# Performance work log

Hardware: AMD Instinct MI355X
Metric: run time of the kernel (lower is better)

The kernel has to match this reference:

```python
import jax, jax.numpy as jnp
import numpy as np

EMB = 300      # LEN_EMB_VECTOR
FH, FO = 200, 200
GH, GO = 200, 200
HH, HO = 200, 3

def _mlp2(x, w1, b1, w2, b2):
    # relu(Linear) -> relu(Linear), torch Linear: y = x @ W.T + b
    h = jax.nn.relu(x @ w1.T + b1)
    return jax.nn.relu(h @ w2.T + b2)

def setup_inputs() -> dict:
    key = jax.random.key(0)
    ks = jax.random.split(key, 16)
    L1, L2 = 8192, 8192
    def lin(k, out_d, in_d):
        kw, kb = jax.random.split(k)
        s = 1.0 / np.sqrt(in_d)
        w = jax.random.uniform(kw, (out_d, in_d), jnp.float32, -s, s)
        b = jax.random.uniform(kb, (out_d,), jnp.float32, -s, s)
        return w, b
    F_w1, F_b1 = lin(ks[0], FH, EMB)
    F_w2, F_b2 = lin(ks[1], FO, FH)
    G_w1, G_b1 = lin(ks[2], GH, 2 * EMB)
    G_w2, G_b2 = lin(ks[3], GO, GH)
    H_w1, H_b1 = lin(ks[4], HH, 2 * GO)
    H_w2, H_b2 = lin(ks[5], HO, HH)
    sen1 = jax.random.normal(ks[6], (L1, EMB), jnp.float32)
    sen2 = jax.random.normal(ks[7], (L2, EMB), jnp.float32)
    return {"sen1": sen1, "sen2": sen2,
            "F_w1": F_w1, "F_b1": F_b1, "F_w2": F_w2, "F_b2": F_b2,
            "G_w1": G_w1, "G_b1": G_b1, "G_w2": G_w2, "G_b2": G_b2,
            "H_w1": H_w1, "H_b1": H_b1, "H_w2": H_w2, "H_b2": H_b2}

def reference(sen1, sen2, F_w1, F_b1, F_w2, F_b2,
              G_w1, G_b1, G_w2, G_b2, H_w1, H_b1, H_w2, H_b2):
    # F projection of every token in both sentences
    Fa = _mlp2(sen1, F_w1, F_b1, F_w2, F_b2)   # [L1, 200]
    Fb = _mlp2(sen2, F_w1, F_b1, F_w2, F_b2)   # [L2, 200]
    # E matrix of dot products: e_ij = Fa_i . Fb_j
    E = jnp.einsum('id,jd->ij', Fa, Fb)        # [L1, L2]
    # beta_i = softmax over j of E[i, :] applied to sen2
    beta = jax.nn.softmax(E, axis=1) @ sen2    # [L1, EMB]
    # alpha_j = softmax over i of E[:, j] applied to sen1
    alpha = jax.nn.softmax(E, axis=0).T @ sen1 # [L2, EMB]
    # G comparison
    v1 = _mlp2(jnp.concatenate([sen1, beta], axis=-1), G_w1, G_b1, G_w2, G_b2)   # [L1, 200]
    v2 = _mlp2(jnp.concatenate([sen2, alpha], axis=-1), G_w1, G_b1, G_w2, G_b2)  # [L2, 200]
    # aggregate: elementwise sums over tokens, then H classifier with softmax
    hx = jnp.concatenate([v1.sum(axis=0), v2.sum(axis=0)])  # [400]
    logits = jax.nn.relu(hx @ H_w1.T + H_b1) @ H_w2.T + H_b2  # [3]
    return jax.nn.softmax(logits)
```

## Files before the change

kernel.cpp:

```cpp
#include <hip/hip_runtime.h>

typedef __attribute__((ext_vector_type(8))) short short8;
typedef __attribute__((ext_vector_type(4))) float f32x4;

__device__ inline ushort f2bf(float f) {
    union { float f; unsigned u; } v{f};
    unsigned r = v.u + 0x7FFF + ((v.u >> 16) & 1);
    return (ushort)(r >> 16);
}
__device__ inline float bf2f(ushort u) {
    union { unsigned u; float f; } v;
    v.u = ((unsigned)u) << 16;
    return v.f;
}

__device__ inline void gload_lds16(const void* g, void* l) {
    __builtin_amdgcn_global_load_lds(
        (const __attribute__((address_space(1))) unsigned int*)(uintptr_t)g,
        (__attribute__((address_space(3))) unsigned int*)(uintptr_t)l,
        16, 0, 0);
}

__global__ __launch_bounds__(256) void convert_sen_kernel(
    const float* __restrict__ s1, const float* __restrict__ s2,
    ushort* __restrict__ Senb, ushort* __restrict__ St1, ushort* __restrict__ St2)
{
    const float* X = blockIdx.z ? s2 : s1;
    ushort* Xt = blockIdx.z ? St2 : St1;
    ushort* Sb = Senb + (size_t)blockIdx.z * 8192 * 320;
    __shared__ float t[64][65];
    const int r0 = blockIdx.x * 64, c0 = blockIdx.y * 64;
    const int tc = threadIdx.x & 63, tr = threadIdx.x >> 6;
    for (int rr = tr; rr < 64; rr += 4) {
        int c = c0 + tc;
        float v = (c < 300) ? X[(size_t)(r0 + rr) * 300 + c] : 0.f;
        t[rr][tc] = v;
        if (c < 320) Sb[(size_t)(r0 + rr) * 320 + c] = f2bf(v);
    }
    __syncthreads();
    for (int rr = tr; rr < 64; rr += 4) {
        int oc = c0 + rr;
        if (oc < 320)
            Xt[(size_t)oc * 8192 + r0 + tc] = f2bf(t[tc][rr]);
    }
}

__global__ __launch_bounds__(256) void convert_weights_kernel(
    const float* __restrict__ W0, const float* __restrict__ b0,
    const float* __restrict__ W1, const float* __restrict__ b1,
    const float* __restrict__ W2, const float* __restrict__ b2,
    const float* __restrict__ W3, const float* __restrict__ b3,
    ushort* __restrict__ Wb0, float* __restrict__ bp0,
    ushort* __restrict__ Wb1, float* __restrict__ bp1,
    ushort* __restrict__ Wb2, float* __restrict__ bp2,
    ushort* __restrict__ Wb3, float* __restrict__ bp3)
{
    const int id = blockIdx.x;
    const int mat = id / 224, n = id % 224;
    if (mat == 2) {
        for (int k = threadIdx.x; k < 640; k += 256) {
            float v = 0.f;
            if (n < 200) {
                if (k < 320) { if (k < 300) v = W2[(size_t)n * 600 + k]; }
                else { int cc = k - 320; if (cc < 300) v = W2[(size_t)n * 600 + 300 + cc]; }
            }
            Wb2[(size_t)n * 640 + k] = f2bf(v);
        }
        if (threadIdx.x == 0) bp2[n] = (n < 200) ? b2[n] : 0.f;
        return;
    }
    const float* W; const float* b; ushort* Wb; float* bp; int N, K, KP;
    if (mat == 0)      { W = W0; b = b0; Wb = Wb0; bp = bp0; N = 200; K = 300; KP = 320; }
    else if (mat == 1) { W = W1; b = b1; Wb = Wb1; bp = bp1; N = 200; K = 200; KP = 224; }
    else               { W = W3; b = b3; Wb = Wb3; bp = bp3; N = 200; K = 200; KP = 224; }
    for (int k = threadIdx.x; k < KP; k += 256)
        Wb[(size_t)n * KP + k] = (n < N && k < K) ? f2bf(W[(size_t)n * K + k]) : (ushort)0;
    if (threadIdx.x == 0) bp[n] = (n < N) ? b[n] : 0.f;
}

__global__ __launch_bounds__(64) void mlp2_kernel(
    const ushort* __restrict__ X, int KP1,
    const ushort* __restrict__ W1, const float* __restrict__ b1,
    const ushort* __restrict__ W2, const float* __restrict__ b2,
    ushort* __restrict__ Ybf)
{
    const int r0 = blockIdx.x * 16;
    const int lane = threadIdx.x;
    const int lr = lane & 15, lg = lane >> 4;

    __shared__ __align__(16) ushort Y1[16][232];

    f32x4 a1[14];
#pragma unroll
    for (int t = 0; t < 14; ++t) a1[t] = f32x4{0.f, 0.f, 0.f, 0.f};

    const ushort* Xrow = X + (size_t)(r0 + lr) * KP1 + lg * 8;
    const ushort* W1r  = W1 + (size_t)lr * KP1 + lg * 8;
    for (int k0 = 0; k0 < KP1; k0 += 32) {
        short8 a = *(const short8*)(Xrow + k0);
#pragma unroll
        for (int t = 0; t < 14; ++t) {
            short8 bfr = *(const short8*)(W1r + (size_t)t * 16 * KP1 + k0);
            a1[t] = __builtin_amdgcn_mfma_f32_16x16x32_bf16(a, bfr, a1[t], 0, 0, 0);
        }
    }
#pragma unroll
    for (int t = 0; t < 14; ++t) {
        int col = t * 16 + lr;
        float bv = b1[col];
#pragma unroll
        for (int rr = 0; rr < 4; ++rr)
            Y1[lg * 4 + rr][col] = f2bf(fmaxf(a1[t][rr] + bv, 0.f));
    }
    __syncthreads();

    f32x4 a2[14];
#pragma unroll
    for (int t = 0; t < 14; ++t) a2[t] = f32x4{0.f, 0.f, 0.f, 0.f};
    const ushort* W2r = W2 + (size_t)lr * 224 + lg * 8;
    for (int k0 = 0; k0 < 224; k0 += 32) {
        short8 a = *(const short8*)&Y1[lr][lg * 8 + k0];
#pragma unroll
        for (int t = 0; t < 14; ++t) {
            short8 bfr = *(const short8*)(W2r + (size_t)t * 16 * 224 + k0);
            a2[t] = __builtin_amdgcn_mfma_f32_16x16x32_bf16(a, bfr, a2[t], 0, 0, 0);
        }
    }
#pragma unroll
    for (int t = 0; t < 14; ++t) {
        int col = t * 16 + lr;
        float bv = b2[col];
#pragma unroll
        for (int rr = 0; rr < 4; ++rr) {
            int row = r0 + lg * 4 + rr;
            Ybf[(size_t)row * 224 + col] = f2bf(fmaxf(a2[t][rr] + bv, 0.f));
        }
    }
}

__global__ __launch_bounds__(64) void gmlp2_kernel(
    const ushort* __restrict__ Senb,
    const ushort* __restrict__ Pacc, const float* __restrict__ Dpart,
    const ushort* __restrict__ W1, const float* __restrict__ b1,
    const ushort* __restrict__ W2, const float* __restrict__ b2,
    float* __restrict__ Part)
{
    const int r0 = blockIdx.x * 16;
    const int lane = threadIdx.x;
    const int lr = lane & 15, lg = lane >> 4;
    const int row = r0 + lr;

    __shared__ __align__(16) ushort Y1[16][232];

    const float inv = 1.f / (Dpart[row] + Dpart[16384 + row]);
    const ushort* pa = Pacc + (size_t)row * 320;
    const ushort* pb = pa + (size_t)16384 * 320;

    f32x4 a1[14];
#pragma unroll
    for (int t = 0; t < 14; ++t) a1[t] = f32x4{0.f, 0.f, 0.f, 0.f};

    const ushort* Xrow = Senb + (size_t)row * 320 + lg * 8;
    const ushort* W1r  = W1 + (size_t)lr * 640 + lg * 8;
    for (int k0 = 0; k0 < 640; k0 += 32) {
        short8 a;
        if (k0 < 320) {
            a = *(const short8*)(Xrow + k0);
        } else {
            int kk = k0 - 320 + lg * 8;
            short8 x = *(const short8*)(pa + kk);
            short8 y = *(const short8*)(pb + kk);
#pragma unroll
            for (int m = 0; m < 8; ++m)
                a[m] = (short)f2bf((bf2f((ushort)x[m]) + bf2f((ushort)y[m])) * inv);
        }
#pragma unroll
        for (int t = 0; t < 14; ++t) {
            short8 bfr = *(const short8*)(W1r + (size_t)t * 16 * 640 + k0);
            a1[t] = __builtin_amdgcn_mfma_f32_16x16x32_bf16(a, bfr, a1[t], 0, 0, 0);
        }
    }
#pragma unroll
    for (int t = 0; t < 14; ++t) {
        int col = t * 16 + lr;
        float bv = b1[col];
#pragma unroll
        for (int rr = 0; rr < 4; ++rr)
            Y1[lg * 4 + rr][col] = f2bf(fmaxf(a1[t][rr] + bv, 0.f));
    }
    __syncthreads();

    f32x4 a2[14];
#pragma unroll
    for (int t = 0; t < 14; ++t) a2[t] = f32x4{0.f, 0.f, 0.f, 0.f};
    const ushort* W2r = W2 + (size_t)lr * 224 + lg * 8;
    for (int k0 = 0; k0 < 224; k0 += 32) {
        short8 a = *(const short8*)&Y1[lr][lg * 8 + k0];
#pragma unroll
        for (int t = 0; t < 14; ++t) {
            short8 bfr = *(const short8*)(W2r + (size_t)t * 16 * 224 + k0);
            a2[t] = __builtin_amdgcn_mfma_f32_16x16x32_bf16(a, bfr, a2[t], 0, 0, 0);
        }
    }
#pragma unroll
    for (int t = 0; t < 14; ++t) {
        int col = t * 16 + lr;
        if (col < 200) {
            float bv = b2[col];
            float s = 0.f;
#pragma unroll
            for (int rr = 0; rr < 4; ++rr)
                s += fmaxf(a2[t][rr] + bv, 0.f);
            s += __shfl_xor(s, 16);
            s += __shfl_xor(s, 32);
            if (lg == 0)
                Part[(size_t)blockIdx.x * 200 + col] = s;
        }
    }
}

__global__ __launch_bounds__(512, 2) void attend_mfma_kernel(
    const ushort* __restrict__ FaFb, const ushort* __restrict__ St1,
    const ushort* __restrict__ St2, ushort* __restrict__ Pacc,
    float* __restrict__ Dpart)
{
    const int b = blockIdx.x;
    const int it  = b & 63;
    const int jh  = (b >> 6) & 1;
    const int dir = b >> 7;
    const ushort* A  = FaFb + (dir ? (size_t)8192 * 224 : 0);
    const ushort* B  = FaFb + (dir ? 0 : (size_t)8192 * 224);
    const ushort* St = dir ? St1 : St2;
    const int ib = it * 128;
    const int jo = jh * 4096;

    const int tid = threadIdx.x;
    const int w = tid >> 6;
    const int wi = w >> 1, wj = w & 1;
    const int dq = w & 3,  ih = w >> 2;
    const int lane = tid & 63;
    const int lr = lane & 15, lg = lane >> 4;

    __shared__ __align__(16) ushort Bl[2][28 * 512];
    __shared__ __align__(16) ushort Sl[2][40 * 512];
    __shared__ __align__(16) ushort Pl[128][76];
    __shared__ float dled[8][32];

    f32x4 acc[4][5];
#pragma unroll
    for (int s = 0; s < 4; ++s)
#pragma unroll
        for (int t = 0; t < 5; ++t) acc[s][t] = f32x4{0.f, 0.f, 0.f, 0.f};
    float dsum[2] = {0.f, 0.f};

    short8 afr[2][7];
#pragma unroll
    for (int si = 0; si < 2; ++si) {
        const ushort* Ar = A + (size_t)(ib + wi * 32 + si * 16 + lr) * 224 + lg * 8;
#pragma unroll
        for (int k = 0; k < 7; ++k) afr[si][k] = *(const short8*)(Ar + k * 32);
    }

    const int nB = (w < 4) ? 4 : 3;
    const int pB = (w < 4) ? (w * 4) : (16 + (w - 4) * 3);
    int boff[4];
#pragma unroll
    for (int q = 0; q < 4; ++q) {
        int p = pB + q;
        boff[q] = ((p / 7) * 16 + lr) * 448 + ((p % 7) * 32 + lg * 8) * 2;
    }
    const char* Bb = (const char*)B + (size_t)jo * 448;

    int soff[5];
#pragma unroll
    for (int q = 0; q < 5; ++q) {
        int p = w * 5 + q;
        int srow = p * 8 + (lane >> 3);
        int sl = (lane & 7) ^ (srow & 7);
        soff[q] = srow * 16384 + sl * 16;
    }
    const char* Sb = (const char*)St + (size_t)jo * 2;

    int prow[5], prow7[5];
#pragma unroll
    for (int t = 0; t < 5; ++t) {
        prow[t] = (dq * 80 + t * 16 + lr) * 128;
        prow7[t] = (dq * 80 + t * 16 + lr) & 7;
    }

#pragma unroll
    for (int q = 0; q < 4; ++q)
        if (q < nB) gload_lds16(Bb + boff[q], &Bl[0][(pB + q) * 512]);
#pragma unroll
    for (int q = 0; q < 5; ++q)
        gload_lds16(Sb + soff[q], &Sl[0][(w * 5 + q) * 512]);
    __syncthreads();

    int buf = 0;
    for (int jb = 0; jb < 4096; jb += 64, buf ^= 1) {
        f32x4 e[2][2];
#pragma unroll
        for (int si = 0; si < 2; ++si)
#pragma unroll
            for (int jt = 0; jt < 2; ++jt) e[si][jt] = f32x4{0.f, 0.f, 0.f, 0.f};
        __builtin_amdgcn_s_setprio(1);
#pragma unroll
        for (int kk = 0; kk < 7; ++kk) {
            short8 b0 = *(const short8*)&Bl[buf][((2 * wj + 0) * 7 + kk) * 512 + lane * 8];
            short8 b1 = *(const short8*)&Bl[buf][((2 * wj + 1) * 7 + kk) * 512 + lane * 8];
            e[0][0] = __builtin_amdgcn_mfma_f32_16x16x32_bf16(b0, afr[0][kk], e[0][0], 0, 0, 0);
            e[1][0] = __builtin_amdgcn_mfma_f32_16x16x32_bf16(b0, afr[1][kk], e[1][0], 0, 0, 0);
            e[0][1] = __builtin_amdgcn_mfma_f32_16x16x32_bf16(b1, afr[0][kk], e[0][1], 0, 0, 0);
            e[1][1] = __builtin_amdgcn_mfma_f32_16x16x32_bf16(b1, afr[1][kk], e[1][1], 0, 0, 0);
        }
        __builtin_amdgcn_s_setprio(0);

#pragma unroll
        for (int si = 0; si < 2; ++si) {
#pragma unroll
            for (int jt = 0; jt < 2; ++jt) {
                float x0 = __expf(e[si][jt][0]);
                float x1 = __expf(e[si][jt][1]);
                float x2 = __expf(e[si][jt][2]);
                float x3 = __expf(e[si][jt][3]);
                dsum[si] += (x0 + x1) + (x2 + x3);
                uint2 pk;
                pk.x = (unsigned)f2bf(x0) | ((unsigned)f2bf(x1) << 16);
                pk.y = (unsigned)f2bf(x2) | ((unsigned)f2bf(x3) << 16);
                *(uint2*)&Pl[wi * 32 + si * 16 + lr][wj * 32 + jt * 16 + lg * 4] = pk;
            }
        }
        __syncthreads();

        if (jb + 64 < 4096) {
            const char* Bn = Bb + (size_t)(jb + 64) * 448;
            const char* Sn = Sb + (size_t)(jb + 64) * 2;
#pragma unroll
            for (int q = 0; q < 4; ++q)
                if (q < nB) gload_lds16(Bn + boff[q], &Bl[buf ^ 1][(pB + q) * 512]);
#pragma unroll
            for (int q = 0; q < 5; ++q)
                gload_lds16(Sn + soff[q], &Sl[buf ^ 1][(w * 5 + q) * 512]);
        }

#pragma unroll
        for (int h = 0; h < 2; ++h) {
            short8 pf[4];
#pragma unroll
            for (int s = 0; s < 4; ++s)
                pf[s] = *(const short8*)&Pl[ih * 64 + s * 16 + lr][h * 32 + lg * 8];
            short8 st[5];
#pragma unroll
            for (int t = 0; t < 5; ++t) {
                int sl = ((h << 2) | lg) ^ prow7[t];
                st[t] = *(const short8*)((const char*)Sl[buf] + prow[t] + (sl << 4));
            }
            __builtin_amdgcn_s_setprio(1);
#pragma unroll
            for (int s = 0; s < 4; ++s)
#pragma unroll
                for (int t = 0; t < 5; ++t)
                    acc[s][t] = __builtin_amdgcn_mfma_f32_16x16x32_bf16(pf[s], st[t], acc[s][t], 0, 0, 0);
            __builtin_amdgcn_s_setprio(0);
        }
        __syncthreads();
    }

#pragma unroll
    for (int si = 0; si < 2; ++si) {
        dsum[si] += __shfl_xor(dsum[si], 16);
        dsum[si] += __shfl_xor(dsum[si], 32);
    }
    if (lg == 0) {
#pragma unroll
        for (int si = 0; si < 2; ++si)
            dled[w][si * 16 + lr] = dsum[si];
    }
    __syncthreads();

    if (tid < 128) {
        int wi2 = tid >> 5, idx = tid & 31;
        Dpart[(size_t)jh * 16384 + dir * 8192 + ib + tid] =
            dled[wi2 * 2][idx] + dled[wi2 * 2 + 1][idx];
    }

    ushort* Pb = Pacc + ((size_t)jh * 16384 + dir * 8192 + ib + ih * 64) * 320;
#pragma unroll
    for (int t = 0; t < 5; ++t) {
        int d = dq * 80 + t * 16 + lr;
#pragma unroll
        for (int s = 0; s < 4; ++s)
#pragma unroll
            for (int r = 0; r < 4; ++r)
                Pb[(size_t)(s * 16 + lg * 4 + r) * 320 + d] = f2bf(acc[s][t][r]);
    }
}

__global__ __launch_bounds__(256) void colsum_part_kernel(
    const float* __restrict__ Part, float* __restrict__ hsum)
{
    const int c = blockIdx.x;
    const int base = (c < 200) ? 0 : 512;
    const int col = c % 200;
    float s = 0.f;
    for (int p = threadIdx.x; p < 512; p += 256)
        s += Part[(size_t)(base + p) * 200 + col];
    __shared__ float red[256];
    red[threadIdx.x] = s;
    __syncthreads();
    for (int off = 128; off > 0; off >>= 1) {
        if (threadIdx.x < off) red[threadIdx.x] += red[threadIdx.x + off];
        __syncthreads();
    }
    if (threadIdx.x == 0) hsum[c] = red[0];
}

__global__ __launch_bounds__(256) void head_kernel(
    const float* __restrict__ hsum,
    const float* __restrict__ Hw1, const float* __restrict__ Hb1,
    const float* __restrict__ Hw2, const float* __restrict__ Hb2,
    float* __restrict__ out)
{
    __shared__ float hx[400];
    __shared__ float hr[200];
    __shared__ float lg[3];
    const int t = threadIdx.x;
    for (int i = t; i < 400; i += 256) hx[i] = hsum[i];
    __syncthreads();
    if (t < 200) {
        float a = Hb1[t];
        for (int k = 0; k < 400; ++k) a = fmaf(hx[k], Hw1[t * 400 + k], a);
        hr[t] = fmaxf(a, 0.f);
    }
    __syncthreads();
    if (t < 3) {
        float a = Hb2[t];
        for (int k = 0; k < 200; ++k) a = fmaf(hr[k], Hw2[t * 200 + k], a);
        lg[t] = a;
    }
    __syncthreads();
    if (t == 0) {
        float m = fmaxf(lg[0], fmaxf(lg[1], lg[2]));
        float e0 = __expf(lg[0] - m);
        float e1 = __expf(lg[1] - m);
        float e2 = __expf(lg[2] - m);
        float s = e0 + e1 + e2;
        out[0] = e0 / s;
        out[1] = e1 / s;
        out[2] = e2 / s;
    }
}

extern "C" void kernel_launch(void* const* d_in, const int* in_sizes, int n_in,
                              void* d_out, int out_size, void* d_ws, size_t ws_size,
                              hipStream_t stream)
{
    const float* sen1 = (const float*)d_in[0];
    const float* sen2 = (const float*)d_in[1];
    const float* F_w1 = (const float*)d_in[2];
    const float* F_b1 = (const float*)d_in[3];
    const float* F_w2 = (const float*)d_in[4];
    const float* F_b2 = (const float*)d_in[5];
    const float* G_w1 = (const float*)d_in[6];
    const float* G_b1 = (const float*)d_in[7];
    const float* G_w2 = (const float*)d_in[8];
    const float* G_b2 = (const float*)d_in[9];
    const float* H_w1 = (const float*)d_in[10];
    const float* H_b1 = (const float*)d_in[11];
    const float* H_w2 = (const float*)d_in[12];
    const float* H_b2 = (const float*)d_in[13];
    float* out = (float*)d_out;

    const int L = 8192;
    char* p = (char*)d_ws;
    ushort* St1  = (ushort*)p; p += (size_t)320 * L * 2;
    ushort* St2  = (ushort*)p; p += (size_t)320 * L * 2;
    ushort* Senb = (ushort*)p; p += (size_t)2 * L * 320 * 2;
    ushort* FaFb = (ushort*)p; p += (size_t)2 * L * 224 * 2;
    ushort* WbF1 = (ushort*)p; p += (size_t)224 * 320 * 2;
    ushort* WbF2 = (ushort*)p; p += (size_t)224 * 224 * 2;
    ushort* WbG1 = (ushort*)p; p += (size_t)224 * 640 * 2;
    ushort* WbG2 = (ushort*)p; p += (size_t)224 * 224 * 2;
    float*  bpF1 = (float*)p;  p += 224 * 4;
    float*  bpF2 = (float*)p;  p += 224 * 4;
    float*  bpG1 = (float*)p;  p += 224 * 4;
    float*  bpG2 = (float*)p;  p += 224 * 4;
    float*  hsum = (float*)p;  p += 400 * 4;
    ushort* Pacc = (ushort*)p; p += (size_t)2 * 16384 * 320 * 2;
    float*  Dpart= (float*)p;  p += (size_t)2 * 16384 * 4;
    float*  Part = (float*)p;  p += (size_t)1024 * 200 * 4;

    dim3 blk256(256);

    hipLaunchKernelGGL(convert_sen_kernel, dim3(L / 64, 5, 2), blk256, 0, stream,
                       sen1, sen2, Senb, St1, St2);
    hipLaunchKernelGGL(convert_weights_kernel, dim3(4 * 224), blk256, 0, stream,
                       F_w1, F_b1, F_w2, F_b2, G_w1, G_b1, G_w2, G_b2,
                       WbF1, bpF1, WbF2, bpF2, WbG1, bpG1, WbG2, bpG2);

    hipLaunchKernelGGL(mlp2_kernel, dim3(2 * L / 16), dim3(64), 0, stream,
                       Senb, 320, WbF1, bpF1, WbF2, bpF2, FaFb);

    hipLaunchKernelGGL(attend_mfma_kernel, dim3(256), dim3(512), 0, stream,
                       FaFb, St1, St2, Pacc, Dpart);

    hipLaunchKernelGGL(gmlp2_kernel, dim3(2 * L / 16), dim3(64), 0, stream,
                       Senb, Pacc, Dpart, WbG1, bpG1, WbG2, bpG2, Part);

    hipLaunchKernelGGL(colsum_part_kernel, dim3(400), blk256, 0, stream, Part, hsum);
    hipLaunchKernelGGL(head_kernel, dim3(1), blk256, 0, stream,
                       hsum, H_w1, H_b1, H_w2, H_b2, out);
}
```

Before: 275.9 us.

## Split MLP K-dimension across two waves and merge prep/tail kernels

The F and G two-layer MLP kernels now run two wavefronts per block, each covering half of the K dimension. Partial sums are exchanged through shared memory, rounded to bf16, before bias and ReLU. The two conversion kernels are merged into one launch, and the column-sum and head kernels are merged into a single 1024-thread tail kernel. The aim is more parallelism in the latency-bound MLPs and fewer launches, at the cost of extra syncs and bf16 rounding of the partial sums.

```diff
diff --git a/kernel.cpp b/kernel.cpp
--- a/kernel.cpp
+++ b/kernel.cpp
@@ -21,15 +21,51 @@
         16, 0, 0);
 }
 
-__global__ __launch_bounds__(256) void convert_sen_kernel(
+__global__ __launch_bounds__(256) void prep_kernel(
     const float* __restrict__ s1, const float* __restrict__ s2,
-    ushort* __restrict__ Senb, ushort* __restrict__ St1, ushort* __restrict__ St2)
+    const float* __restrict__ W0, const float* __restrict__ b0,
+    const float* __restrict__ W1, const float* __restrict__ b1,
+    const float* __restrict__ W2, const float* __restrict__ b2,
+    const float* __restrict__ W3, const float* __restrict__ b3,
+    ushort* __restrict__ Senb, ushort* __restrict__ St1, ushort* __restrict__ St2,
+    ushort* __restrict__ Wb0, float* __restrict__ bp0,
+    ushort* __restrict__ Wb1, float* __restrict__ bp1,
+    ushort* __restrict__ Wb2, float* __restrict__ bp2,
+    ushort* __restrict__ Wb3, float* __restrict__ bp3)
 {
-    const float* X = blockIdx.z ? s2 : s1;
-    ushort* Xt = blockIdx.z ? St2 : St1;
-    ushort* Sb = Senb + (size_t)blockIdx.z * 8192 * 320;
+    const int bid = blockIdx.x;
+    if (bid < 896) {
+        const int mat = bid / 224, n = bid % 224;
+        if (mat == 2) {
+            for (int k = threadIdx.x; k < 640; k += 256) {
+                float v = 0.f;
+                if (n < 200) {
+                    if (k < 320) { if (k < 300) v = W2[(size_t)n * 600 + k]; }
+                    else { int cc = k - 320; if (cc < 300) v = W2[(size_t)n * 600 + 300 + cc]; }
+                }
+                Wb2[(size_t)n * 640 + k] = f2bf(v);
+            }
+            if (threadIdx.x == 0) bp2[n] = (n < 200) ? b2[n] : 0.f;
+            return;
+        }
+        const float* W; const float* b; ushort* Wb; float* bp; int N, K, KP;
+        if (mat == 0)      { W = W0; b = b0; Wb = Wb0; bp = bp0; N = 200; K = 300; KP = 320; }
+        else if (mat == 1) { W = W1; b = b1; Wb = Wb1; bp = bp1; N = 200; K = 200; KP = 224; }
+        else               { W = W3; b = b3; Wb = Wb3; bp = bp3; N = 200; K = 200; KP = 224; }
+        for (int k = threadIdx.x; k < KP; k += 256)
+            Wb[(size_t)n * KP + k] = (n < N && k < K) ? f2bf(W[(size_t)n * K + k]) : (ushort)0;
+        if (threadIdx.x == 0) bp[n] = (n < N) ? b[n] : 0.f;
+        return;
+    }
+    const int sb = bid - 896;
+    const int gx = sb & 127;
+    const int rest = sb >> 7;
+    const int gy = rest % 5, gz = rest / 5;
+    const float* X = gz ? s2 : s1;
+    ushort* Xt = gz ? St2 : St1;
+    ushort* Sb = Senb + (size_t)gz * 8192 * 320;
     __shared__ float t[64][65];
-    const int r0 = blockIdx.x * 64, c0 = blockIdx.y * 64;
+    const int r0 = gx * 64, c0 = gy * 64;
     const int tc = threadIdx.x & 63, tr = threadIdx.x >> 6;
     for (int rr = tr; rr < 64; rr += 4) {
         int c = c0 + tc;
@@ -45,72 +81,55 @@
     }
 }
 
-__global__ __launch_bounds__(256) void convert_weights_kernel(
-    const float* __restrict__ W0, const float* __restrict__ b0,
-    const float* __restrict__ W1, const float* __restrict__ b1,
-    const float* __restrict__ W2, const float* __restrict__ b2,
-    const float* __restrict__ W3, const float* __restrict__ b3,
-    ushort* __restrict__ Wb0, float* __restrict__ bp0,
-    ushort* __restrict__ Wb1, float* __restrict__ bp1,
-    ushort* __restrict__ Wb2, float* __restrict__ bp2,
-    ushort* __restrict__ Wb3, float* __restrict__ bp3)
-{
-    const int id = blockIdx.x;
-    const int mat = id / 224, n = id % 224;
-    if (mat == 2) {
-        for (int k = threadIdx.x; k < 640; k += 256) {
-            float v = 0.f;
-            if (n < 200) {
-                if (k < 320) { if (k < 300) v = W2[(size_t)n * 600 + k]; }
-                else { int cc = k - 320; if (cc < 300) v = W2[(size_t)n * 600 + 300 + cc]; }
-            }
-            Wb2[(size_t)n * 640 + k] = f2bf(v);
-        }
-        if (threadIdx.x == 0) bp2[n] = (n < 200) ? b2[n] : 0.f;
-        return;
-    }
-    const float* W; const float* b; ushort* Wb; float* bp; int N, K, KP;
-    if (mat == 0)      { W = W0; b = b0; Wb = Wb0; bp = bp0; N = 200; K = 300; KP = 320; }
-    else if (mat == 1) { W = W1; b = b1; Wb = Wb1; bp = bp1; N = 200; K = 200; KP = 224; }
-    else               { W = W3; b = b3; Wb = Wb3; bp = bp3; N = 200; K = 200; KP = 224; }
-    for (int k = threadIdx.x; k < KP; k += 256)
-        Wb[(size_t)n * KP + k] = (n < N && k < K) ? f2bf(W[(size_t)n * K + k]) : (ushort)0;
-    if (threadIdx.x == 0) bp[n] = (n < N) ? b[n] : 0.f;
-}
-
-__global__ __launch_bounds__(64) void mlp2_kernel(
-    const ushort* __restrict__ X, int KP1,
+__global__ __launch_bounds__(128) void mlp2_kernel(
+    const ushort* __restrict__ X,
     const ushort* __restrict__ W1, const float* __restrict__ b1,
     const ushort* __restrict__ W2, const float* __restrict__ b2,
     ushort* __restrict__ Ybf)
 {
     const int r0 = blockIdx.x * 16;
-    const int lane = threadIdx.x;
+    const int tid = threadIdx.x;
+    const int wv = tid >> 6;
+    const int lane = tid & 63;
     const int lr = lane & 15, lg = lane >> 4;
 
     __shared__ __align__(16) ushort Y1[16][232];
+    __shared__ __align__(16) ushort Pp[16][224];
 
     f32x4 a1[14];
 #pragma unroll
     for (int t = 0; t < 14; ++t) a1[t] = f32x4{0.f, 0.f, 0.f, 0.f};
 
-    const ushort* Xrow = X + (size_t)(r0 + lr) * KP1 + lg * 8;
-    const ushort* W1r  = W1 + (size_t)lr * KP1 + lg * 8;
-    for (int k0 = 0; k0 < KP1; k0 += 32) {
+    const ushort* Xrow = X + (size_t)(r0 + lr) * 320 + lg * 8;
+    const ushort* W1r  = W1 + (size_t)lr * 320 + lg * 8;
+    const int kb1 = wv * 160;
+    for (int k0 = kb1; k0 < kb1 + 160; k0 += 32) {
         short8 a = *(const short8*)(Xrow + k0);
 #pragma unroll
         for (int t = 0; t < 14; ++t) {
-            short8 bfr = *(const short8*)(W1r + (size_t)t * 16 * KP1 + k0);
+            short8 bfr = *(const short8*)(W1r + (size_t)t * 16 * 320 + k0);
             a1[t] = __builtin_amdgcn_mfma_f32_16x16x32_bf16(a, bfr, a1[t], 0, 0, 0);
         }
     }
-#pragma unroll
-    for (int t = 0; t < 14; ++t) {
-        int col = t * 16 + lr;
-        float bv = b1[col];
-#pragma unroll
-        for (int rr = 0; rr < 4; ++rr)
-            Y1[lg * 4 + rr][col] = f2bf(fmaxf(a1[t][rr] + bv, 0.f));
+    if (wv == 1) {
+#pragma unroll
+        for (int t = 0; t < 14; ++t)
+#pragma unroll
+            for (int rr = 0; rr < 4; ++rr)
+                Pp[lg * 4 + rr][t * 16 + lr] = f2bf(a1[t][rr]);
+    }
+    __syncthreads();
+    if (wv == 0) {
+#pragma unroll
+        for (int t = 0; t < 14; ++t) {
+            int col = t * 16 + lr;
+            float bv = b1[col];
+#pragma unroll
+            for (int rr = 0; rr < 4; ++rr) {
+                float v = a1[t][rr] + bf2f(Pp[lg * 4 + rr][col]) + bv;
+                Y1[lg * 4 + rr][col] = f2bf(fmaxf(v, 0.f));
+            }
+        }
     }
     __syncthreads();
 
@@ -118,7 +137,8 @@
 #pragma unroll
     for (int t = 0; t < 14; ++t) a2[t] = f32x4{0.f, 0.f, 0.f, 0.f};
     const ushort* W2r = W2 + (size_t)lr * 224 + lg * 8;
-    for (int k0 = 0; k0 < 224; k0 += 32) {
+    const int kb2 = wv * 128, ke2 = wv ? 224 : 128;
+    for (int k0 = kb2; k0 < ke2; k0 += 32) {
         short8 a = *(const short8*)&Y1[lr][lg * 8 + k0];
 #pragma unroll
         for (int t = 0; t < 14; ++t) {
@@ -126,19 +146,30 @@
             a2[t] = __builtin_amdgcn_mfma_f32_16x16x32_bf16(a, bfr, a2[t], 0, 0, 0);
         }
     }
-#pragma unroll
-    for (int t = 0; t < 14; ++t) {
-        int col = t * 16 + lr;
-        float bv = b2[col];
-#pragma unroll
-        for (int rr = 0; rr < 4; ++rr) {
-            int row = r0 + lg * 4 + rr;
-            Ybf[(size_t)row * 224 + col] = f2bf(fmaxf(a2[t][rr] + bv, 0.f));
-        }
-    }
-}
-
-__global__ __launch_bounds__(64) void gmlp2_kernel(
+    if (wv == 1) {
+#pragma unroll
+        for (int t = 0; t < 14; ++t)
+#pragma unroll
+            for (int rr = 0; rr < 4; ++rr)
+                Pp[lg * 4 + rr][t * 16 + lr] = f2bf(a2[t][rr]);
+    }
+    __syncthreads();
+    if (wv == 0) {
+#pragma unroll
+        for (int t = 0; t < 14; ++t) {
+            int col = t * 16 + lr;
+            float bv = b2[col];
+#pragma unroll
+            for (int rr = 0; rr < 4; ++rr) {
+                int row = r0 + lg * 4 + rr;
+                float v = a2[t][rr] + bf2f(Pp[lg * 4 + rr][col]) + bv;
+                Ybf[(size_t)row * 224 + col] = f2bf(fmaxf(v, 0.f));
+            }
+        }
+    }
+}
+
+__global__ __launch_bounds__(128) void gmlp2_kernel(
     const ushort* __restrict__ Senb,
     const ushort* __restrict__ Pacc, const float* __restrict__ Dpart,
     const ushort* __restrict__ W1, const float* __restrict__ b1,
@@ -146,47 +177,68 @@
     float* __restrict__ Part)
 {
     const int r0 = blockIdx.x * 16;
-    const int lane = threadIdx.x;
+    const int tid = threadIdx.x;
+    const int wv = tid >> 6;
+    const int lane = tid & 63;
     const int lr = lane & 15, lg = lane >> 4;
     const int row = r0 + lr;
 
     __shared__ __align__(16) ushort Y1[16][232];
-
-    const float inv = 1.f / (Dpart[row] + Dpart[16384 + row]);
-    const ushort* pa = Pacc + (size_t)row * 320;
-    const ushort* pb = pa + (size_t)16384 * 320;
+    __shared__ __align__(16) ushort Pp[16][224];
 
     f32x4 a1[14];
 #pragma unroll
     for (int t = 0; t < 14; ++t) a1[t] = f32x4{0.f, 0.f, 0.f, 0.f};
 
-    const ushort* Xrow = Senb + (size_t)row * 320 + lg * 8;
-    const ushort* W1r  = W1 + (size_t)lr * 640 + lg * 8;
-    for (int k0 = 0; k0 < 640; k0 += 32) {
-        short8 a;
-        if (k0 < 320) {
-            a = *(const short8*)(Xrow + k0);
-        } else {
+    const ushort* W1r = W1 + (size_t)lr * 640 + lg * 8;
+    if (wv == 0) {
+        const ushort* Xrow = Senb + (size_t)row * 320 + lg * 8;
+        for (int k0 = 0; k0 < 320; k0 += 32) {
+            short8 a = *(const short8*)(Xrow + k0);
+#pragma unroll
+            for (int t = 0; t < 14; ++t) {
+                short8 bfr = *(const short8*)(W1r + (size_t)t * 16 * 640 + k0);
+                a1[t] = __builtin_amdgcn_mfma_f32_16x16x32_bf16(a, bfr, a1[t], 0, 0, 0);
+            }
+        }
+    } else {
+        const float inv = 1.f / (Dpart[row] + Dpart[16384 + row]);
+        const ushort* pa = Pacc + (size_t)row * 320;
+        const ushort* pb = pa + (size_t)16384 * 320;
+        for (int k0 = 320; k0 < 640; k0 += 32) {
             int kk = k0 - 320 + lg * 8;
             short8 x = *(const short8*)(pa + kk);
             short8 y = *(const short8*)(pb + kk);
+            short8 a;
 #pragma unroll
             for (int m = 0; m < 8; ++m)
                 a[m] = (short)f2bf((bf2f((ushort)x[m]) + bf2f((ushort)y[m])) * inv);
-        }
-#pragma unroll
-        for (int t = 0; t < 14; ++t) {
-            short8 bfr = *(const short8*)(W1r + (size_t)t * 16 * 640 + k0);
-            a1[t] = __builtin_amdgcn_mfma_f32_16x16x32_bf16(a, bfr, a1[t], 0, 0, 0);
-        }
-    }
-#pragma unroll
-    for (int t = 0; t < 14; ++t) {
-        int col = t * 16 + lr;
-        float bv = b1[col];
-#pragma unroll
-        for (int rr = 0; rr < 4; ++rr)
-            Y1[lg * 4 + rr][col] = f2bf(fmaxf(a1[t][rr] + bv, 0.f));
+#pragma unroll
+            for (int t = 0; t < 14; ++t) {
+                short8 bfr = *(const short8*)(W1r + (size_t)t * 16 * 640 + k0);
+                a1[t] = __builtin_amdgcn_mfma_f32_16x16x32_bf16(a, bfr, a1[t], 0, 0, 0);
+            }
+        }
+    }
+    if (wv == 1) {
+#pragma unroll
+        for (int t = 0; t < 14; ++t)
+#pragma unroll
+            for (int rr = 0; rr < 4; ++rr)
+                Pp[lg * 4 + rr][t * 16 + lr] = f2bf(a1[t][rr]);
+    }
+    __syncthreads();
+    if (wv == 0) {
+#pragma unroll
+        for (int t = 0; t < 14; ++t) {
+            int col = t * 16 + lr;
+            float bv = b1[col];
+#pragma unroll
+            for (int rr = 0; rr < 4; ++rr) {
+                float v = a1[t][rr] + bf2f(Pp[lg * 4 + rr][col]) + bv;
+                Y1[lg * 4 + rr][col] = f2bf(fmaxf(v, 0.f));
+            }
+        }
     }
     __syncthreads();
 
@@ -194,7 +246,8 @@
 #pragma unroll
     for (int t = 0; t < 14; ++t) a2[t] = f32x4{0.f, 0.f, 0.f, 0.f};
     const ushort* W2r = W2 + (size_t)lr * 224 + lg * 8;
-    for (int k0 = 0; k0 < 224; k0 += 32) {
+    const int kb2 = wv * 128, ke2 = wv ? 224 : 128;
+    for (int k0 = kb2; k0 < ke2; k0 += 32) {
         short8 a = *(const short8*)&Y1[lr][lg * 8 + k0];
 #pragma unroll
         for (int t = 0; t < 14; ++t) {
@@ -202,19 +255,31 @@
             a2[t] = __builtin_amdgcn_mfma_f32_16x16x32_bf16(a, bfr, a2[t], 0, 0, 0);
         }
     }
-#pragma unroll
-    for (int t = 0; t < 14; ++t) {
-        int col = t * 16 + lr;
-        if (col < 200) {
-            float bv = b2[col];
-            float s = 0.f;
+    if (wv == 1) {
+#pragma unroll
+        for (int t = 0; t < 14; ++t)
 #pragma unroll
             for (int rr = 0; rr < 4; ++rr)
-                s += fmaxf(a2[t][rr] + bv, 0.f);
-            s += __shfl_xor(s, 16);
-            s += __shfl_xor(s, 32);
-            if (lg == 0)
-                Part[(size_t)blockIdx.x * 200 + col] = s;
+                Pp[lg * 4 + rr][t * 16 + lr] = f2bf(a2[t][rr]);
+    }
+    __syncthreads();
+    if (wv == 0) {
+#pragma unroll
+        for (int t = 0; t < 14; ++t) {
+            int col = t * 16 + lr;
+            if (col < 200) {
+                float bv = b2[col];
+                float s = 0.f;
+#pragma unroll
+                for (int rr = 0; rr < 4; ++rr) {
+                    float v = a2[t][rr] + bf2f(Pp[lg * 4 + rr][col]) + bv;
+                    s += fmaxf(v, 0.f);
+                }
+                s += __shfl_xor(s, 16);
+                s += __shfl_xor(s, 32);
+                if (lg == 0)
+                    Part[(size_t)blockIdx.x * 200 + col] = s;
+            }
         }
     }
 }
@@ -396,54 +461,59 @@
     }
 }
 
-__global__ __launch_bounds__(256) void colsum_part_kernel(
-    const float* __restrict__ Part, float* __restrict__ hsum)
-{
-    const int c = blockIdx.x;
-    const int base = (c < 200) ? 0 : 512;
-    const int col = c % 200;
-    float s = 0.f;
-    for (int p = threadIdx.x; p < 512; p += 256)
-        s += Part[(size_t)(base + p) * 200 + col];
-    __shared__ float red[256];
-    red[threadIdx.x] = s;
-    __syncthreads();
-    for (int off = 128; off > 0; off >>= 1) {
-        if (threadIdx.x < off) red[threadIdx.x] += red[threadIdx.x + off];
-        __syncthreads();
-    }
-    if (threadIdx.x == 0) hsum[c] = red[0];
-}
-
-__global__ __launch_bounds__(256) void head_kernel(
-    const float* __restrict__ hsum,
+__global__ __launch_bounds__(1024) void tail_kernel(
+    const float* __restrict__ Part,
     const float* __restrict__ Hw1, const float* __restrict__ Hb1,
     const float* __restrict__ Hw2, const float* __restrict__ Hb2,
     float* __restrict__ out)
 {
+    __shared__ float hpart[800];
     __shared__ float hx[400];
     __shared__ float hr[200];
-    __shared__ float lg[3];
-    const int t = threadIdx.x;
-    for (int i = t; i < 400; i += 256) hx[i] = hsum[i];
-    __syncthreads();
-    if (t < 200) {
-        float a = Hb1[t];
-        for (int k = 0; k < 400; ++k) a = fmaf(hx[k], Hw1[t * 400 + k], a);
-        hr[t] = fmaxf(a, 0.f);
-    }
-    __syncthreads();
-    if (t < 3) {
-        float a = Hb2[t];
-        for (int k = 0; k < 200; ++k) a = fmaf(hr[k], Hw2[t * 200 + k], a);
-        lg[t] = a;
-    }
-    __syncthreads();
-    if (t == 0) {
-        float m = fmaxf(lg[0], fmaxf(lg[1], lg[2]));
-        float e0 = __expf(lg[0] - m);
-        float e1 = __expf(lg[1] - m);
-        float e2 = __expf(lg[2] - m);
+    __shared__ float lgts[3];
+    const int tid = threadIdx.x;
+
+    if (tid < 800) {
+        int oc = tid >> 1, ph = tid & 1;
+        const float* base = Part + ((size_t)((oc < 200 ? 0 : 512) + ph * 256)) * 200 + (oc % 200);
+        float s = 0.f;
+        for (int q = 0; q < 256; ++q) s += base[(size_t)q * 200];
+        hpart[tid] = s;
+    }
+    __syncthreads();
+    if (tid < 400) hx[tid] = hpart[2 * tid] + hpart[2 * tid + 1];
+    __syncthreads();
+
+    {
+        int r = tid >> 2, p = tid & 3;
+        float a = 0.f;
+        if (r < 200) {
+            for (int kk = 0; kk < 100; ++kk) {
+                int k = p + 4 * kk;
+                a = fmaf(hx[k], Hw1[r * 400 + k], a);
+            }
+        }
+        a += __shfl_xor(a, 1);
+        a += __shfl_xor(a, 2);
+        if (p == 0 && r < 200) hr[r] = fmaxf(a + Hb1[r], 0.f);
+    }
+    __syncthreads();
+
+    if (tid < 192) {
+        int o = tid >> 6, ln = tid & 63;
+        float a = 0.f;
+        for (int k = ln; k < 200; k += 64)
+            a = fmaf(hr[k], Hw2[o * 200 + k], a);
+#pragma unroll
+        for (int m = 1; m < 64; m <<= 1) a += __shfl_xor(a, m);
+        if (ln == 0) lgts[o] = a + Hb2[o];
+    }
+    __syncthreads();
+    if (tid == 0) {
+        float m = fmaxf(lgts[0], fmaxf(lgts[1], lgts[2]));
+        float e0 = __expf(lgts[0] - m);
+        float e1 = __expf(lgts[1] - m);
+        float e2 = __expf(lgts[2] - m);
         float s = e0 + e1 + e2;
         out[0] = e0 / s;
         out[1] = e1 / s;
@@ -485,29 +555,25 @@
     float*  bpF2 = (float*)p;  p += 224 * 4;
     float*  bpG1 = (float*)p;  p += 224 * 4;
     float*  bpG2 = (float*)p;  p += 224 * 4;
-    float*  hsum = (float*)p;  p += 400 * 4;
     ushort* Pacc = (ushort*)p; p += (size_t)2 * 16384 * 320 * 2;
     float*  Dpart= (float*)p;  p += (size_t)2 * 16384 * 4;
     float*  Part = (float*)p;  p += (size_t)1024 * 200 * 4;
 
-    dim3 blk256(256);
-
-    hipLaunchKernelGGL(convert_sen_kernel, dim3(L / 64, 5, 2), blk256, 0, stream,
-                       sen1, sen2, Senb, St1, St2);
-    hipLaunchKernelGGL(convert_weights_kernel, dim3(4 * 224), blk256, 0, stream,
+    hipLaunchKernelGGL(prep_kernel, dim3(896 + 1280), dim3(256), 0, stream,
+                       sen1, sen2,
                        F_w1, F_b1, F_w2, F_b2, G_w1, G_b1, G_w2, G_b2,
+                       Senb, St1, St2,
                        WbF1, bpF1, WbF2, bpF2, WbG1, bpG1, WbG2, bpG2);
 
-    hipLaunchKernelGGL(mlp2_kernel, dim3(2 * L / 16), dim3(64), 0, stream,
-                       Senb, 320, WbF1, bpF1, WbF2, bpF2, FaFb);
+    hipLaunchKernelGGL(mlp2_kernel, dim3(2 * L / 16), dim3(128), 0, stream,
+                       Senb, WbF1, bpF1, WbF2, bpF2, FaFb);
 
     hipLaunchKernelGGL(attend_mfma_kernel, dim3(256), dim3(512), 0, stream,
                        FaFb, St1, St2, Pacc, Dpart);
 
-    hipLaunchKernelGGL(gmlp2_kernel, dim3(2 * L / 16), dim3(64), 0, stream,
+    hipLaunchKernelGGL(gmlp2_kernel, dim3(2 * L / 16), dim3(128), 0, stream,
                        Senb, Pacc, Dpart, WbG1, bpG1, WbG2, bpG2, Part);
 
-    hipLaunchKernelGGL(colsum_part_kernel, dim3(400), blk256, 0, stream, Part, hsum);
-    hipLaunchKernelGGL(head_kernel, dim3(1), blk256, 0, stream,
-                       hsum, H_w1, H_b1, H_w2, H_b2, out);
-}
+    hipLaunchKernelGGL(tail_kernel, dim3(1), dim3(1024), 0, stream,
+                       Part, H_w1, H_b1, H_w2, H_b2, out);
+}
```

Result: no change. 280.2 us (+1.6%).
